# Optimization experiments

Hardware: AMD Instinct MI355X
Metric: run time of the kernel (lower is better)

The kernel has to match this reference:

```python
import jax, jax.numpy as jnp
import numpy as np

EPS = 1e-5

def _ln(x, w, b):
    mu = jnp.mean(x, -1, keepdims=True)
    var = jnp.mean((x - mu) ** 2, -1, keepdims=True)
    return (x - mu) * jax.lax.rsqrt(var + EPS) * w + b

def setup_inputs() -> dict:
    key = jax.random.key(0)
    ks = jax.random.split(key, 12)
    B, H, W, C = 4, 32, 32, 768
    nh, hd, hidden = 12, 64, 3072
    s = lambda k, sh, fan: jax.random.normal(k, sh, jnp.float32) * (fan ** -0.5)
    return {
        "x": jax.random.normal(ks[0], (B, H, W, C), jnp.float32),
        "norm1_w": jnp.ones((C,), jnp.float32),
        "norm1_b": jnp.zeros((C,), jnp.float32),
        "qkv_w": s(ks[1], (C, 3 * C), C),
        "qkv_b": jnp.zeros((3 * C,), jnp.float32),
        "proj_w": s(ks[2], (C, C), C),
        "proj_b": jnp.zeros((C,), jnp.float32),
        "rel_h": jnp.ones((2 * H - 1, hd), jnp.float32),
        "rel_w": jnp.ones((2 * W - 1, hd), jnp.float32),
        "norm2_w": jnp.ones((C,), jnp.float32),
        "norm2_b": jnp.zeros((C,), jnp.float32),
        "mlp_w1": s(ks[3], (C, hidden), C),
        "mlp_b1": jnp.zeros((hidden,), jnp.float32),
        "mlp_w2": s(ks[4], (hidden, C), hidden),
        "mlp_b2": jnp.zeros((C,), jnp.float32),
    }

def reference(x, norm1_w, norm1_b, qkv_w, qkv_b, proj_w, proj_b, rel_h, rel_w,
              norm2_w, norm2_b, mlp_w1, mlp_b1, mlp_w2, mlp_b2):
    B, H, W, C = x.shape
    nh = 12
    hd = C // nh
    scale = hd ** -0.5
    S = H * W

    xn = _ln(x, norm1_w, norm1_b)
    qkv = (xn.reshape(B, S, C) @ qkv_w + qkv_b)            # [B,S,3C]
    qkv = qkv.reshape(B, S, 3, nh, hd).transpose(2, 0, 3, 1, 4).reshape(3, B * nh, S, hd)
    q, k, v = qkv[0], qkv[1], qkv[2]                        # [B*nh,S,hd]

    attn = jnp.einsum('bqd,bkd->bqk', q * scale, k)         # [B*nh,S,S]

    # relative position bias (q_size == k_size == H or W)
    idx_h = jnp.arange(H)[:, None] - jnp.arange(H)[None, :] + (H - 1)
    idx_w = jnp.arange(W)[:, None] - jnp.arange(W)[None, :] + (W - 1)
    Rh = rel_h[idx_h]                                       # [H,H,hd]
    Rw = rel_w[idx_w]                                       # [W,W,hd]
    q4 = q.reshape(B * nh, H, W, hd)                        # unscaled q, as in source
    bias_h = jnp.einsum('bhwc,hkc->bhwk', q4, Rh)           # [B*nh,H,W,H]
    bias_w = jnp.einsum('bhwc,wkc->bhwk', q4, Rw)           # [B*nh,H,W,W]
    attn = (attn.reshape(B * nh, H, W, H, W)
            + bias_h[:, :, :, :, None]
            + bias_w[:, :, :, None, :]).reshape(B * nh, S, S)

    attn = jax.nn.softmax(attn, axis=-1)
    out = jnp.einsum('bqk,bkd->bqd', attn, v)               # [B*nh,S,hd]
    out = out.reshape(B, nh, H, W, hd).transpose(0, 2, 3, 1, 4).reshape(B, H, W, C)
    x = out @ proj_w + proj_b + x

    xn = _ln(x, norm2_w, norm2_b)
    h = jax.nn.gelu(xn @ mlp_w1 + mlp_b1, approximate=False)
    return h @ mlp_w2 + mlp_b2 + x
```

## Files before the change

### kernel.cpp

```cpp
#include <hip/hip_runtime.h>
#include <hip/hip_bf16.h>
#include <cstdint>
#include <cstddef>

typedef __bf16 bf16x8 __attribute__((ext_vector_type(8)));
typedef float  f32x4  __attribute__((ext_vector_type(4)));
typedef unsigned short u16x8 __attribute__((ext_vector_type(8)));

#define S_TOT 1024
#define NH 12
#define HD 64
#define NBH 48
#define CDIM 768

static __device__ __forceinline__ unsigned short f2bf(float f) {
    unsigned int u = __builtin_bit_cast(unsigned int, f);
    u += 0x7FFFu + ((u >> 16) & 1u);
    return (unsigned short)(u >> 16);
}

static __device__ __forceinline__ void async16(void* lds, const void* g) {
    __builtin_amdgcn_global_load_lds(
        (const __attribute__((address_space(1))) unsigned int*)g,
        (__attribute__((address_space(3))) unsigned int*)lds, 16, 0, 0);
}

static __device__ __forceinline__ int xcd_swz(int orig, int nwg) {
    return (orig & 7) * (nwg >> 3) + (orig >> 3);
}

__launch_bounds__(256)
__global__ void ln_kernel(const float* __restrict__ x, const float* __restrict__ w,
                          const float* __restrict__ b, unsigned short* __restrict__ out)
{
    const int row = blockIdx.x;
    const int tid = threadIdx.x;
    const float* xr = x + (size_t)row * CDIM;
    float v0 = xr[tid], v1 = xr[tid + 256], v2 = xr[tid + 512];
    float s  = v0 + v1 + v2;
    float s2 = v0 * v0 + v1 * v1 + v2 * v2;
    #pragma unroll
    for (int off = 32; off > 0; off >>= 1) {
        s  += __shfl_xor(s,  off);
        s2 += __shfl_xor(s2, off);
    }
    __shared__ float ss[4], ss2[4];
    const int wid = tid >> 6;
    if ((tid & 63) == 0) { ss[wid] = s; ss2[wid] = s2; }
    __syncthreads();
    s  = ss[0] + ss[1] + ss[2] + ss[3];
    s2 = ss2[0] + ss2[1] + ss2[2] + ss2[3];
    const float mu  = s * (1.0f / CDIM);
    const float var = s2 * (1.0f / CDIM) - mu * mu;
    const float rs  = rsqrtf(var + 1e-5f);
    unsigned short* orow = out + (size_t)row * CDIM;
    float vv[3] = {v0, v1, v2};
    #pragma unroll
    for (int i = 0; i < 3; ++i) {
        int c = tid + i * 256;
        orow[c] = f2bf((vv[i] - mu) * rs * w[c] + b[c]);
    }
}

__launch_bounds__(256)
__global__ void wt_kernel(const float* __restrict__ W, unsigned short* __restrict__ WT,
                          int K, int N)
{
    __shared__ float tile[32][33];
    const int k0 = blockIdx.x * 32, n0 = blockIdx.y * 32;
    const int tx = threadIdx.x & 31, ty = threadIdx.x >> 5;
    #pragma unroll
    for (int i = 0; i < 4; ++i) {
        int kk = ty + i * 8;
        tile[kk][tx] = W[(size_t)(k0 + kk) * N + n0 + tx];
    }
    __syncthreads();
    #pragma unroll
    for (int i = 0; i < 4; ++i) {
        int nn = ty + i * 8;
        WT[(size_t)(n0 + nn) * K + k0 + tx] = f2bf(tile[tx][nn]);
    }
}

__launch_bounds__(256)
__global__ void vtrans_kernel(const unsigned short* __restrict__ v,
                              unsigned short* __restrict__ vT)
{
    __shared__ unsigned short tile[64][65];
    const int bh = blockIdx.x;
    const int s0 = blockIdx.y * 64;
    const int tid = threadIdx.x;
    #pragma unroll
    for (int it = 0; it < 2; ++it) {
        int idx = tid + it * 256;
        int r = idx >> 3, c0 = (idx & 7) * 8;
        *(u16x8*)&tile[r][c0] = *(const u16x8*)&v[((size_t)bh * S_TOT + s0 + r) * HD + c0];
    }
    __syncthreads();
    #pragma unroll
    for (int it = 0; it < 2; ++it) {
        int idx = tid + it * 256;
        int d = idx >> 3, sc = (idx & 7) * 8;
        u16x8 o;
        #pragma unroll
        for (int e = 0; e < 8; ++e) o[e] = tile[sc + e][d];
        *(u16x8*)&vT[((size_t)bh * HD + d) * S_TOT + s0 + sc] = o;
    }
}

template<int EPI>
__launch_bounds__(256)
__global__ void gemm_kernel(const unsigned short* __restrict__ A,
                            const unsigned short* __restrict__ BT,
                            const float* __restrict__ bias,
                            const float* __restrict__ res,
                            float* __restrict__ outf,
                            unsigned short* __restrict__ outh,
                            int M, int N, int K)
{
    __shared__ __align__(16) unsigned short As[128 * 64];
    __shared__ __align__(16) unsigned short Bs[128 * 64];
    const int tid  = threadIdx.x;
    const int nwgx = gridDim.x;
    const int wg   = xcd_swz(blockIdx.y * nwgx + blockIdx.x, nwgx * gridDim.y);
    const int bm   = (wg % nwgx) * 128;
    const int bn   = (wg / nwgx) * 128;
    const int wid  = tid >> 6, lane = tid & 63;
    const int wr   = (wid >> 1) * 64, wc = (wid & 1) * 64;
    const int fr   = lane & 15, fk = lane >> 4;

    f32x4 acc[4][4] = {};

    for (int kk = 0; kk < K; kk += 64) {
        __syncthreads();
        #pragma unroll
        for (int it = 0; it < 4; ++it) {
            int idx = tid + it * 256;
            int r = idx >> 3;
            int j = (idx & 7) ^ (r & 7);
            async16(&As[idx * 8], &A[(size_t)(bm + r) * K + kk + j * 8]);
            async16(&Bs[idx * 8], &BT[(size_t)(bn + r) * K + kk + j * 8]);
        }
        __syncthreads();
        #pragma unroll
        for (int ks = 0; ks < 2; ++ks) {
            bf16x8 af[4], bfv[4];
            #pragma unroll
            for (int i = 0; i < 4; ++i) {
                int Ra = wr + i * 16 + fr;
                af[i]  = *(const bf16x8*)&As[Ra * 64 + (((ks * 4 + fk) ^ (Ra & 7)) * 8)];
                int Rb = wc + i * 16 + fr;
                bfv[i] = *(const bf16x8*)&Bs[Rb * 64 + (((ks * 4 + fk) ^ (Rb & 7)) * 8)];
            }
            __builtin_amdgcn_s_setprio(1);
            #pragma unroll
            for (int i = 0; i < 4; ++i)
                #pragma unroll
                for (int j = 0; j < 4; ++j)
                    acc[i][j] = __builtin_amdgcn_mfma_f32_16x16x32_bf16(af[i], bfv[j], acc[i][j], 0, 0, 0);
            __builtin_amdgcn_s_setprio(0);
        }
    }

    const int er = (lane >> 4) * 4;
    const int ec = lane & 15;
    #pragma unroll
    for (int i = 0; i < 4; ++i) {
        const int rowb = bm + wr + i * 16 + er;
        #pragma unroll
        for (int j = 0; j < 4; ++j) {
            const int col = bn + wc + j * 16 + ec;
            #pragma unroll
            for (int r = 0; r < 4; ++r) {
                const int row = rowb + r;
                float val = acc[i][j][r] + bias[col];
                if constexpr (EPI == 0) {
                    int bb = row >> 10, s = row & 1023;
                    int t  = col / CDIM;
                    int rem = col - t * CDIM;
                    int hh = rem >> 6, d = rem & 63;
                    outh[((size_t)(t * NBH + bb * NH + hh) * S_TOT + s) * HD + d] = f2bf(val);
                } else if constexpr (EPI == 1) {
                    size_t idx = (size_t)row * N + col;
                    outf[idx] = val + res[idx];
                } else {
                    float g = 0.5f * val * (1.0f + erff(val * 0.70710678f));
                    outh[(size_t)row * N + col] = f2bf(g);
                }
            }
        }
    }
}

__launch_bounds__(256)
__global__ void gemm64_kernel(const unsigned short* __restrict__ A,
                              const unsigned short* __restrict__ BT,
                              const float* __restrict__ bias,
                              const float* __restrict__ res,
                              float* __restrict__ outf,
                              int M, int N, int K)
{
    __shared__ __align__(16) unsigned short As[64 * 64];
    __shared__ __align__(16) unsigned short Bs[64 * 64];
    const int tid  = threadIdx.x;
    const int nwgx = gridDim.x;
    const int wg   = xcd_swz(blockIdx.y * nwgx + blockIdx.x, nwgx * gridDim.y);
    const int bm   = (wg % nwgx) * 64;
    const int bn   = (wg / nwgx) * 64;
    const int wid  = tid >> 6, lane = tid & 63;
    const int wr   = (wid >> 1) * 32, wc = (wid & 1) * 32;
    const int fr   = lane & 15, fk = lane >> 4;

    f32x4 acc[2][2] = {};

    for (int kk = 0; kk < K; kk += 64) {
        __syncthreads();
        #pragma unroll
        for (int it = 0; it < 2; ++it) {
            int idx = tid + it * 256;
            int r = idx >> 3;
            int j = (idx & 7) ^ (r & 7);
            async16(&As[idx * 8], &A[(size_t)(bm + r) * K + kk + j * 8]);
            async16(&Bs[idx * 8], &BT[(size_t)(bn + r) * K + kk + j * 8]);
        }
        __syncthreads();
        #pragma unroll
        for (int ks = 0; ks < 2; ++ks) {
            bf16x8 af[2], bfv[2];
            #pragma unroll
            for (int i = 0; i < 2; ++i) {
                int Ra = wr + i * 16 + fr;
                af[i]  = *(const bf16x8*)&As[Ra * 64 + (((ks * 4 + fk) ^ (Ra & 7)) * 8)];
                int Rb = wc + i * 16 + fr;
                bfv[i] = *(const bf16x8*)&Bs[Rb * 64 + (((ks * 4 + fk) ^ (Rb & 7)) * 8)];
            }
            __builtin_amdgcn_s_setprio(1);
            #pragma unroll
            for (int i = 0; i < 2; ++i)
                #pragma unroll
                for (int j = 0; j < 2; ++j)
                    acc[i][j] = __builtin_amdgcn_mfma_f32_16x16x32_bf16(af[i], bfv[j], acc[i][j], 0, 0, 0);
            __builtin_amdgcn_s_setprio(0);
        }
    }

    const int er = (lane >> 4) * 4;
    const int ec = lane & 15;
    #pragma unroll
    for (int i = 0; i < 2; ++i) {
        const int rowb = bm + wr + i * 16 + er;
        #pragma unroll
        for (int j = 0; j < 2; ++j) {
            const int col = bn + wc + j * 16 + ec;
            #pragma unroll
            for (int r = 0; r < 4; ++r) {
                const int row = rowb + r;
                size_t idx = (size_t)row * N + col;
                outf[idx] = acc[i][j][r] + bias[col] + res[idx];
            }
        }
    }
}

__launch_bounds__(256)
__global__ void bias_kernel(const unsigned short* __restrict__ q,
                            const float* __restrict__ rel_h,
                            const float* __restrict__ rel_w,
                            float* __restrict__ biasH,
                            float* __restrict__ biasW)
{
    __shared__ __align__(16) unsigned short Bl[32 * 72];
    const int tid  = threadIdx.x;
    const int wid  = tid >> 6, lane = tid & 63;
    const int fr   = lane & 15, fk = lane >> 4;
    const int mt   = blockIdx.x;
    const int qc   = blockIdx.y;
    const int mode = blockIdx.z;
    const float* rel = mode ? rel_w : rel_h;
    float* outp = mode ? biasW : biasH;

    {
        int row = tid >> 3, c0 = (tid & 7) * 8;
        const float* rp = rel + (size_t)(qc + 31 - row) * HD + c0;
        u16x8 o;
        #pragma unroll
        for (int e = 0; e < 8; ++e) o[e] = f2bf(rp[e]);
        *(u16x8*)&Bl[row * 72 + c0] = o;
    }
    __syncthreads();

    const int ri = wid * 16 + fr;
    const int bh = mt * 2 + (ri >> 5);
    const int inner = ri & 31;
    const int s = mode ? (inner * 32 + qc) : (qc * 32 + inner);
    const unsigned short* arow = q + ((size_t)bh * S_TOT + s) * HD;

    f32x4 acc[2] = {};
    #pragma unroll
    for (int ks = 0; ks < 2; ++ks) {
        bf16x8 af = *(const bf16x8*)&arow[ks * 32 + fk * 8];
        #pragma unroll
        for (int nt = 0; nt < 2; ++nt) {
            bf16x8 bfv = *(const bf16x8*)&Bl[(nt * 16 + fr) * 72 + ks * 32 + fk * 8];
            acc[nt] = __builtin_amdgcn_mfma_f32_16x16x32_bf16(af, bfv, acc[nt], 0, 0, 0);
        }
    }

    const int g = lane >> 4, c = lane & 15;
    #pragma unroll
    for (int reg = 0; reg < 4; ++reg) {
        int ro = wid * 16 + g * 4 + reg;
        int bho = mt * 2 + (ro >> 5);
        int io  = ro & 31;
        int so  = mode ? (io * 32 + qc) : (qc * 32 + io);
        float* op = outp + ((size_t)bho * S_TOT + so) * 32;
        op[c]      = acc[0][reg];
        op[16 + c] = acc[1][reg];
    }
}

__launch_bounds__(256, 4)
__global__ void attn_kernel(const unsigned short* __restrict__ qkv,
                            const unsigned short* __restrict__ vT,
                            const float* __restrict__ biasH,
                            const float* __restrict__ biasW,
                            unsigned short* __restrict__ out)
{
    __shared__ __align__(16) unsigned short Ks[64 * 64];
    __shared__ __align__(16) unsigned short Vt[64 * 64];
    __shared__ __align__(16) unsigned short Pst[4][16][72];

    const int tid  = threadIdx.x;
    const int wid  = tid >> 6;
    const int lane = tid & 63;
    const int fr   = lane & 15, fk = lane >> 4;
    const int er   = (lane >> 4) * 4, ec = lane & 15;
    const int bh_  = blockIdx.x % NBH;
    const int qt   = blockIdx.x / NBH;
    const int row0 = qt * 64;
    const int b    = bh_ / NH, h = bh_ - b * NH;

    const unsigned short* q = qkv;
    const unsigned short* k = qkv + (size_t)NBH * S_TOT * HD;
    const size_t headoff  = (size_t)bh_ * S_TOT * HD;
    const size_t vheadoff = (size_t)bh_ * HD * S_TOT;

    #pragma unroll
    for (int it = 0; it < 2; ++it) {
        int idx = tid + it * 256;
        int r = idx >> 3;
        int j = (idx & 7) ^ (r & 7);
        async16(&Ks[idx * 8], &q[headoff + (size_t)(row0 + r) * HD + j * 8]);
    }
    __syncthreads();

    bf16x8 qf[2];
    {
        int Rq = wid * 16 + fr;
        qf[0] = *(const bf16x8*)&Ks[Rq * 64 + ((fk ^ (Rq & 7)) * 8)];
        qf[1] = *(const bf16x8*)&Ks[Rq * 64 + (((4 + fk) ^ (Rq & 7)) * 8)];
    }

    float bh0[4], bh1[4], bw0[4], bw1[4];
    {
        const int g = lane >> 4, c = lane & 15;
        #pragma unroll
        for (int reg = 0; reg < 4; ++reg) {
            int rt = row0 + wid * 16 + g * 4 + reg;
            const float* ph = biasH + ((size_t)bh_ * S_TOT + rt) * 32;
            const float* pw = biasW + ((size_t)bh_ * S_TOT + rt) * 32;
            bh0[reg] = ph[c];  bh1[reg] = ph[16 + c];
            bw0[reg] = pw[c];  bw1[reg] = pw[16 + c];
        }
    }

    const u16x8 ones_u = {0x3F80, 0x3F80, 0x3F80, 0x3F80, 0x3F80, 0x3F80, 0x3F80, 0x3F80};
    const bf16x8 ones = __builtin_bit_cast(bf16x8, ones_u);

    float m[4], l[4];
    f32x4 oacc[4];
    #pragma unroll
    for (int r = 0; r < 4; ++r) {
        m[r] = -1e30f; l[r] = 0.f;
        oacc[r][0] = 0.f; oacc[r][1] = 0.f; oacc[r][2] = 0.f; oacc[r][3] = 0.f;
    }

    for (int kt = 0; kt < 16; ++kt) {
        __syncthreads();
        #pragma unroll
        for (int it = 0; it < 2; ++it) {
            int idx = tid + it * 256;
            int r = idx >> 3;
            int j = (idx & 7) ^ (r & 7);
            async16(&Ks[idx * 8], &k[headoff + (size_t)(kt * 64 + r) * HD + j * 8]);
            async16(&Vt[idx * 8], &vT[vheadoff + (size_t)r * S_TOT + kt * 64 + j * 8]);
        }
        __syncthreads();

        f32x4 sacc[4] = {};
        __builtin_amdgcn_s_setprio(1);
        #pragma unroll
        for (int nt = 0; nt < 4; ++nt) {
            int Rk = nt * 16 + fr;
            bf16x8 b0 = *(const bf16x8*)&Ks[Rk * 64 + ((fk ^ (Rk & 7)) * 8)];
            bf16x8 b1 = *(const bf16x8*)&Ks[Rk * 64 + (((4 + fk) ^ (Rk & 7)) * 8)];
            sacc[nt] = __builtin_amdgcn_mfma_f32_16x16x32_bf16(qf[0], b0, sacc[nt], 0, 0, 0);
            sacc[nt] = __builtin_amdgcn_mfma_f32_16x16x32_bf16(qf[1], b1, sacc[nt], 0, 0, 0);
        }
        __builtin_amdgcn_s_setprio(0);

        float bhv[2][4];
        #pragma unroll
        for (int j = 0; j < 2; ++j) {
            int kh = kt * 2 + j;
            int src = ((lane >> 4) << 4) + (kh & 15);
            #pragma unroll
            for (int reg = 0; reg < 4; ++reg)
                bhv[j][reg] = (kh < 16) ? __shfl(bh0[reg], src) : __shfl(bh1[reg], src);
        }

        float tmax[4] = {-1e30f, -1e30f, -1e30f, -1e30f};
        #pragma unroll
        for (int nt = 0; nt < 4; ++nt) {
            #pragma unroll
            for (int reg = 0; reg < 4; ++reg) {
                float s_ = sacc[nt][reg] * 0.125f + bhv[nt >> 1][reg]
                         + ((nt & 1) ? bw1[reg] : bw0[reg]);
                sacc[nt][reg] = s_;
                tmax[reg] = fmaxf(tmax[reg], s_);
            }
        }
        #pragma unroll
        for (int reg = 0; reg < 4; ++reg) {
            #pragma unroll
            for (int off = 8; off > 0; off >>= 1)
                tmax[reg] = fmaxf(tmax[reg], __shfl_xor(tmax[reg], off));
            float mnew = fmaxf(m[reg], tmax[reg]);
            float c = __expf(m[reg] - mnew);
            m[reg] = mnew;
            #pragma unroll
            for (int nt = 0; nt < 4; ++nt) {
                float p = __expf(sacc[nt][reg] - mnew);
                Pst[wid][er + reg][nt * 16 + ec] = f2bf(p);
            }
            l[reg] *= c;
            #pragma unroll
            for (int nt = 0; nt < 4; ++nt) oacc[nt][reg] *= c;
        }

        __builtin_amdgcn_s_setprio(1);
        bf16x8 pa0 = *(const bf16x8*)&Pst[wid][fr][fk * 8];
        bf16x8 pa1 = *(const bf16x8*)&Pst[wid][fr][32 + fk * 8];
        f32x4 ps = {};
        ps = __builtin_amdgcn_mfma_f32_16x16x32_bf16(pa0, ones, ps, 0, 0, 0);
        ps = __builtin_amdgcn_mfma_f32_16x16x32_bf16(pa1, ones, ps, 0, 0, 0);
        #pragma unroll
        for (int nt = 0; nt < 4; ++nt) {
            int Rv = nt * 16 + fr;
            bf16x8 vb0 = *(const bf16x8*)&Vt[Rv * 64 + ((fk ^ (Rv & 7)) * 8)];
            bf16x8 vb1 = *(const bf16x8*)&Vt[Rv * 64 + (((4 + fk) ^ (Rv & 7)) * 8)];
            oacc[nt] = __builtin_amdgcn_mfma_f32_16x16x32_bf16(pa0, vb0, oacc[nt], 0, 0, 0);
            oacc[nt] = __builtin_amdgcn_mfma_f32_16x16x32_bf16(pa1, vb1, oacc[nt], 0, 0, 0);
        }
        __builtin_amdgcn_s_setprio(0);
        #pragma unroll
        for (int reg = 0; reg < 4; ++reg) l[reg] += ps[reg];
    }

    #pragma unroll
    for (int reg = 0; reg < 4; ++reg) {
        float inv = 1.0f / l[reg];
        int srow = row0 + wid * 16 + er + reg;
        #pragma unroll
        for (int nt = 0; nt < 4; ++nt) {
            out[((size_t)(b * S_TOT + srow)) * CDIM + h * HD + nt * 16 + ec] =
                f2bf(oacc[nt][reg] * inv);
        }
    }
}

extern "C" void kernel_launch(void* const* d_in, const int* in_sizes, int n_in,
                              void* d_out, int out_size, void* d_ws, size_t ws_size,
                              hipStream_t stream)
{
    const float* x      = (const float*)d_in[0];
    const float* n1w    = (const float*)d_in[1];
    const float* n1b    = (const float*)d_in[2];
    const float* qkv_w  = (const float*)d_in[3];
    const float* qkv_b  = (const float*)d_in[4];
    const float* proj_w = (const float*)d_in[5];
    const float* proj_b = (const float*)d_in[6];
    const float* rel_h  = (const float*)d_in[7];
    const float* rel_w  = (const float*)d_in[8];
    const float* n2w    = (const float*)d_in[9];
    const float* n2b    = (const float*)d_in[10];
    const float* w1     = (const float*)d_in[11];
    const float* b1     = (const float*)d_in[12];
    const float* w2     = (const float*)d_in[13];
    const float* b2     = (const float*)d_in[14];

    char* ws = (char*)d_ws;
    unsigned short* qkvbf = (unsigned short*)(ws + 0);
    float*          biasH = (float*)(ws + 18874368);
    float*          biasW = (float*)(ws + 25165824);
    unsigned short* hbf   = (unsigned short*)(ws + 0);
    float*          x1    = (float*)(ws + 25165824);
    unsigned short* xnbf  = (unsigned short*)(ws + 37748736);
    unsigned short* vTbuf = (unsigned short*)(ws + 37748736);
    unsigned short* wTq   = (unsigned short*)(ws + 44040192);
    unsigned short* wTp   = (unsigned short*)(ws + 47579136);
    unsigned short* wT1   = (unsigned short*)(ws + 48758784);
    unsigned short* wT2   = (unsigned short*)(ws + 53477376);
    unsigned short* aout  = (unsigned short*)(ws + 58195968);

    wt_kernel<<<dim3(768 / 32, 2304 / 32), 256, 0, stream>>>(qkv_w, wTq, 768, 2304);
    wt_kernel<<<dim3(768 / 32, 768 / 32),  256, 0, stream>>>(proj_w, wTp, 768, 768);
    wt_kernel<<<dim3(768 / 32, 3072 / 32), 256, 0, stream>>>(w1, wT1, 768, 3072);
    wt_kernel<<<dim3(3072 / 32, 768 / 32), 256, 0, stream>>>(w2, wT2, 3072, 768);

    ln_kernel<<<4096, 256, 0, stream>>>(x, n1w, n1b, xnbf);
    gemm_kernel<0><<<dim3(32, 18), 256, 0, stream>>>(xnbf, wTq, qkv_b, nullptr, nullptr, qkvbf, 4096, 2304, 768);
    vtrans_kernel<<<dim3(48, 16), 256, 0, stream>>>(qkvbf + (size_t)2 * NBH * S_TOT * HD, vTbuf);
    bias_kernel<<<dim3(24, 32, 2), 256, 0, stream>>>(qkvbf, rel_h, rel_w, biasH, biasW);
    attn_kernel<<<768, 256, 0, stream>>>(qkvbf, vTbuf, biasH, biasW, aout);
    gemm64_kernel<<<dim3(64, 12), 256, 0, stream>>>(aout, wTp, proj_b, x, x1, 4096, 768, 768);
    ln_kernel<<<4096, 256, 0, stream>>>(x1, n2w, n2b, xnbf);
    gemm_kernel<2><<<dim3(32, 24), 256, 0, stream>>>(xnbf, wT1, b1, nullptr, nullptr, hbf, 4096, 3072, 768);
    gemm64_kernel<<<dim3(64, 12), 256, 0, stream>>>(hbf, wT2, b2, x1, (float*)d_out, 4096, 768, 3072);
}
```

Before: 201.9 us.

## Use exp2 softmax with lazy rescaling and merge weight-transpose launches

Folds log2(e) into the attention scale and the precomputed relative-position biases so the online softmax can use exp2f. It also skips the running-max update and accumulator rescale when the new tile max stays within a threshold of the old max, which is checked wave-wide. Separately, the four weight transpose launches become one kernel that picks its matrix from the block index, cutting launch overhead. Lazy rescaling lets probabilities exceed one before normalization, which could reduce bf16 precision of P.

```diff
diff --git a/kernel.cpp b/kernel.cpp
--- a/kernel.cpp
+++ b/kernel.cpp
@@ -12,6 +12,7 @@
 #define HD 64
 #define NBH 48
 #define CDIM 768
+#define L2E 1.44269504088896f
 
 static __device__ __forceinline__ unsigned short f2bf(float f) {
     unsigned int u = __builtin_bit_cast(unsigned int, f);
@@ -63,11 +64,19 @@
 }
 
 __launch_bounds__(256)
-__global__ void wt_kernel(const float* __restrict__ W, unsigned short* __restrict__ WT,
-                          int K, int N)
+__global__ void wt_all_kernel(const float* __restrict__ qkv_w, const float* __restrict__ proj_w,
+                              const float* __restrict__ w1, const float* __restrict__ w2,
+                              unsigned short* __restrict__ wTq, unsigned short* __restrict__ wTp,
+                              unsigned short* __restrict__ wT1, unsigned short* __restrict__ wT2)
 {
     __shared__ float tile[32][33];
-    const int k0 = blockIdx.x * 32, n0 = blockIdx.y * 32;
+    int id = blockIdx.x;
+    const float* W; unsigned short* WT; int K, N, ko, no;
+    if (id < 1728)      { W = qkv_w;  WT = wTq; K = 768;  N = 2304;            ko = id % 24; no = id / 24; }
+    else if (id < 2304) { W = proj_w; WT = wTp; K = 768;  N = 768;  id -= 1728; ko = id % 24; no = id / 24; }
+    else if (id < 4608) { W = w1;     WT = wT1; K = 768;  N = 3072; id -= 2304; ko = id % 24; no = id / 24; }
+    else                { W = w2;     WT = wT2; K = 3072; N = 768;  id -= 4608; ko = id % 96; no = id / 96; }
+    const int k0 = ko * 32, n0 = no * 32;
     const int tx = threadIdx.x & 31, ty = threadIdx.x >> 5;
     #pragma unroll
     for (int i = 0; i < 4; ++i) {
@@ -314,8 +323,8 @@
         int io  = ro & 31;
         int so  = mode ? (io * 32 + qc) : (qc * 32 + io);
         float* op = outp + ((size_t)bho * S_TOT + so) * 32;
-        op[c]      = acc[0][reg];
-        op[16 + c] = acc[1][reg];
+        op[c]      = acc[0][reg] * L2E;
+        op[16 + c] = acc[1][reg] * L2E;
     }
 }
 
@@ -376,6 +385,7 @@
 
     const u16x8 ones_u = {0x3F80, 0x3F80, 0x3F80, 0x3F80, 0x3F80, 0x3F80, 0x3F80, 0x3F80};
     const bf16x8 ones = __builtin_bit_cast(bf16x8, ones_u);
+    const float SCL = 0.125f * L2E;
 
     float m[4], l[4];
     f32x4 oacc[4];
@@ -424,7 +434,7 @@
         for (int nt = 0; nt < 4; ++nt) {
             #pragma unroll
             for (int reg = 0; reg < 4; ++reg) {
-                float s_ = sacc[nt][reg] * 0.125f + bhv[nt >> 1][reg]
+                float s_ = sacc[nt][reg] * SCL + bhv[nt >> 1][reg]
                          + ((nt & 1) ? bw1[reg] : bw0[reg]);
                 sacc[nt][reg] = s_;
                 tmax[reg] = fmaxf(tmax[reg], s_);
@@ -435,17 +445,35 @@
             #pragma unroll
             for (int off = 8; off > 0; off >>= 1)
                 tmax[reg] = fmaxf(tmax[reg], __shfl_xor(tmax[reg], off));
-            float mnew = fmaxf(m[reg], tmax[reg]);
-            float c = __expf(m[reg] - mnew);
-            m[reg] = mnew;
-            #pragma unroll
-            for (int nt = 0; nt < 4; ++nt) {
-                float p = __expf(sacc[nt][reg] - mnew);
-                Pst[wid][er + reg][nt * 16 + ec] = f2bf(p);
-            }
-            l[reg] *= c;
-            #pragma unroll
-            for (int nt = 0; nt < 4; ++nt) oacc[nt][reg] *= c;
+        }
+
+        bool small = true;
+        #pragma unroll
+        for (int reg = 0; reg < 4; ++reg) small = small && (tmax[reg] <= m[reg] + 10.0f);
+        if (__all(small)) {
+            #pragma unroll
+            for (int reg = 0; reg < 4; ++reg) {
+                #pragma unroll
+                for (int nt = 0; nt < 4; ++nt) {
+                    float p = exp2f(sacc[nt][reg] - m[reg]);
+                    Pst[wid][er + reg][nt * 16 + ec] = f2bf(p);
+                }
+            }
+        } else {
+            #pragma unroll
+            for (int reg = 0; reg < 4; ++reg) {
+                float mnew = fmaxf(m[reg], tmax[reg]);
+                float c = exp2f(m[reg] - mnew);
+                m[reg] = mnew;
+                #pragma unroll
+                for (int nt = 0; nt < 4; ++nt) {
+                    float p = exp2f(sacc[nt][reg] - mnew);
+                    Pst[wid][er + reg][nt * 16 + ec] = f2bf(p);
+                }
+                l[reg] *= c;
+                #pragma unroll
+                for (int nt = 0; nt < 4; ++nt) oacc[nt][reg] *= c;
+            }
         }
 
         __builtin_amdgcn_s_setprio(1);
@@ -513,10 +541,7 @@
     unsigned short* wT2   = (unsigned short*)(ws + 53477376);
     unsigned short* aout  = (unsigned short*)(ws + 58195968);
 
-    wt_kernel<<<dim3(768 / 32, 2304 / 32), 256, 0, stream>>>(qkv_w, wTq, 768, 2304);
-    wt_kernel<<<dim3(768 / 32, 768 / 32),  256, 0, stream>>>(proj_w, wTp, 768, 768);
-    wt_kernel<<<dim3(768 / 32, 3072 / 32), 256, 0, stream>>>(w1, wT1, 768, 3072);
-    wt_kernel<<<dim3(3072 / 32, 768 / 32), 256, 0, stream>>>(w2, wT2, 3072, 768);
+    wt_all_kernel<<<6912, 256, 0, stream>>>(qkv_w, proj_w, w1, w2, wTq, wTp, wT1, wT2);
 
     ln_kernel<<<4096, 256, 0, stream>>>(x, n1w, n1b, xnbf);
     gemm_kernel<0><<<dim3(32, 18), 256, 0, stream>>>(xnbf, wTq, qkv_b, nullptr, nullptr, qkvbf, 4096, 2304, 768);
```

New measurement: 198.4 us. About the same (-1.7%).
